# Kernel tuning notes

Measured on AMD Instinct MI355X. Metric: run time of the kernel, lower is better.

The kernel has to match this reference:

```python
import jax, jax.numpy as jnp
import numpy as np

NH, NKV, D = 16, 4, 64
E, NG, TKG, TOPK = 64, 8, 4, 8
RSF = 2.5
EPS = 1e-6
THETA = 10000.0

def rmsnorm(x, w, eps=EPS):
    v = jnp.mean(jnp.square(x.astype(jnp.float32)), axis=-1, keepdims=True)
    return (x * jax.lax.rsqrt(v + eps)).astype(x.dtype) * w

def rope_neox(x, pos):
    # x: [T, heads, D]; neox-style rotation over full head_dim
    d = x.shape[-1]
    inv = 1.0 / (THETA ** (jnp.arange(0, d, 2, dtype=jnp.float32) / d))
    f = pos.astype(jnp.float32)[:, None] * inv              # [T, d/2]
    cos = jnp.cos(f)[:, None, :]
    sin = jnp.sin(f)[:, None, :]
    x1, x2 = jnp.split(x, 2, axis=-1)
    return jnp.concatenate([x1 * cos - x2 * sin, x2 * cos + x1 * sin], axis=-1)


def setup_inputs() -> dict:
    key = jax.random.key(0)
    ks = jax.random.split(key, 12)
    T, H, I, IS = 2048, 1024, 256, 512
    s = 0.02
    return {
        "x": jax.random.normal(ks[0], (T, H), jnp.float32),
        "positions": jnp.arange(T, dtype=jnp.int32),
        "ln1_w": jnp.ones((H,), jnp.float32),
        "w_qkv": jax.random.normal(ks[1], (H, (NH + 2 * NKV) * D), jnp.float32) * s,
        "w_o": jax.random.normal(ks[2], (NH * D, H), jnp.float32) * s,
        "ln2_w": jnp.ones((H,), jnp.float32),
        "gate_w": jax.random.normal(ks[3], (E, H), jnp.float32) * s,
        "expert_bias": jax.random.normal(ks[4], (E,), jnp.float32) * 0.01,
        "we_gate": jax.random.normal(ks[5], (E, H, I), jnp.float32) * s,
        "we_up": jax.random.normal(ks[6], (E, H, I), jnp.float32) * s,
        "we_down": jax.random.normal(ks[7], (E, I, H), jnp.float32) * s,
        "ws_gate_up": jax.random.normal(ks[8], (H, 2 * IS), jnp.float32) * s,
        "ws_down": jax.random.normal(ks[9], (IS, H), jnp.float32) * s,
    }


def reference(x, positions, ln1_w, w_qkv, w_o, ln2_w, gate_w, expert_bias,
              we_gate, we_up, we_down, ws_gate_up, ws_down):
    T, H = x.shape
    residual = x
    # --- attention ---
    h = rmsnorm(x, ln1_w)
    qkv = h @ w_qkv
    q, k, v = jnp.split(qkv, [NH * D, (NH + NKV) * D], axis=-1)
    q = rope_neox(q.reshape(T, NH, D), positions)
    k = rope_neox(k.reshape(T, NKV, D), positions)
    v = v.reshape(T, NKV, D)
    rep = NH // NKV
    k = jnp.repeat(k, rep, axis=1)
    v = jnp.repeat(v, rep, axis=1)
    scores = jnp.einsum('thd,shd->hts', q, k) * (D ** -0.5)
    causal = positions[:, None] >= positions[None, :]
    scores = jnp.where(causal[None], scores, jnp.float32(-1e30))
    p = jax.nn.softmax(scores, axis=-1)
    attn = jnp.einsum('hts,shd->thd', p, v).reshape(T, NH * D)
    residual = residual + attn @ w_o
    # --- MoE block ---
    h = rmsnorm(residual, ln2_w)
    logits = h.astype(jnp.float32) @ gate_w.astype(jnp.float32).T      # [T,E]
    s = jax.nn.sigmoid(logits)
    sc = s + expert_bias[None, :]                                      # bias-corrected scores
    # grouped top-k: score each group by sum of its top-2 corrected scores
    gsc = sc.reshape(T, NG, E // NG)
    group_scores = jax.lax.top_k(gsc, 2)[0].sum(-1)                    # [T,NG]
    _, gidx = jax.lax.top_k(group_scores, TKG)
    gmask = jnp.zeros((T, NG), bool).at[jnp.arange(T)[:, None], gidx].set(True)
    sc_masked = jnp.where(jnp.repeat(gmask, E // NG, axis=1), sc, -jnp.inf)
    _, ids = jax.lax.top_k(sc_masked, TOPK)                            # [T,k]
    w = jnp.take_along_axis(s, ids, axis=-1)                           # weights from raw sigmoid scores
    w = w / (w.sum(-1, keepdims=True) + 1e-20)
    w = w * RSF
    combine = jnp.zeros((T, E), jnp.float32).at[jnp.arange(T)[:, None], ids].add(w)
    combine = combine.astype(h.dtype)
    # routed experts (dense-over-experts reference of the grouped-GEMM dispatch)
    g = jnp.einsum('th,ehi->tei', h, we_gate)
    u = jnp.einsum('th,ehi->tei', h, we_up)
    act = jax.nn.silu(g) * u
    y = jnp.einsum('tei,eih,te->th', act, we_down, combine)
    # shared expert (SwiGLU)
    gu = h @ ws_gate_up
    gs, us = jnp.split(gu, 2, axis=-1)
    y = y + (jax.nn.silu(gs) * us) @ ws_down
    return residual + y
```

## Files before the change

### kernel.cpp

```cpp
#include <hip/hip_runtime.h>
#include <hip/hip_bf16.h>
#include <math.h>

#define T_TOK 2048
#define H_DIM 1024
#define NHH 16
#define NKVH 4
#define HD 64
#define QKV_N 1536
#define NE 64
#define NGRP 8
#define TKG 4
#define TOPKK 8
#define EI 256
#define ISH 512
#define NPOS (T_TOK * TOPKK)

typedef __bf16 bf16_t;
typedef bf16_t bf16x8 __attribute__((ext_vector_type(8)));
typedef bf16_t bf16x4v __attribute__((ext_vector_type(4)));
typedef float f32x4 __attribute__((ext_vector_type(4)));

#define MFMA_BF16 __builtin_amdgcn_mfma_f32_16x16x32_bf16

__global__ void rmsnorm_k(const float* __restrict__ x, const float* __restrict__ w,
                          float* __restrict__ outf, bf16_t* __restrict__ outb) {
  const int t = blockIdx.x;
  const int tid = threadIdx.x;
  const float* xp = x + (size_t)t * H_DIM;
  const float4 x4 = *(const float4*)(xp + tid * 4);
  float s = x4.x * x4.x + x4.y * x4.y + x4.z * x4.z + x4.w * x4.w;
#pragma unroll
  for (int off = 32; off >= 1; off >>= 1) s += __shfl_xor(s, off);
  __shared__ float red[4];
  if ((tid & 63) == 0) red[tid >> 6] = s;
  __syncthreads();
  const float tot = red[0] + red[1] + red[2] + red[3];
  const float r = rsqrtf(tot / (float)H_DIM + 1e-6f);
  const float4 w4 = *(const float4*)(w + tid * 4);
  float4 o;
  o.x = x4.x * r * w4.x; o.y = x4.y * r * w4.y;
  o.z = x4.z * r * w4.z; o.w = x4.w * r * w4.w;
  if (outf) *(float4*)(outf + (size_t)t * H_DIM + tid * 4) = o;
  bf16x4v ob;
  ob[0] = (bf16_t)o.x; ob[1] = (bf16_t)o.y; ob[2] = (bf16_t)o.z; ob[3] = (bf16_t)o.w;
  *(bf16x4v*)(outb + (size_t)t * H_DIM + tid * 4) = ob;
}

__global__ void castT_k(const float* __restrict__ src, bf16_t* __restrict__ dst,
                        int R, int C, size_t srcStride, size_t dstStride,
                        int dstLD, int rowOff) {
  const int e = blockIdx.z;
  const float* sp = src + (size_t)e * srcStride;
  bf16_t* dp = dst + (size_t)e * dstStride;
  const int r0 = blockIdx.y * 32, c0 = blockIdx.x * 32;
  const int tid = threadIdx.x;
  __shared__ float tl[32][33];
  {
    const int rr = tid >> 3, cc4 = (tid & 7) * 4;
    const float4 v = *(const float4*)(sp + (size_t)(r0 + rr) * C + c0 + cc4);
    tl[rr][cc4 + 0] = v.x; tl[rr][cc4 + 1] = v.y;
    tl[rr][cc4 + 2] = v.z; tl[rr][cc4 + 3] = v.w;
  }
  __syncthreads();
  {
    const int cc = tid >> 3, rr4 = (tid & 7) * 4;
    bf16x4v o;
#pragma unroll
    for (int i = 0; i < 4; i++) o[i] = (bf16_t)tl[rr4 + i][cc];
    *(bf16x4v*)(dp + (size_t)(rowOff + c0 + cc) * dstLD + r0 + rr4) = o;
  }
}

__global__ __launch_bounds__(256) void mfma_gemm_k(
    const bf16_t* __restrict__ A, const bf16_t* __restrict__ Bt,
    const float* __restrict__ add0, const float* __restrict__ add1,
    float* __restrict__ C, int M, int N, int K) {
  __shared__ bf16_t Al[128 * 64];
  __shared__ bf16_t Bl[128 * 64];
  const int tid = threadIdx.x;
  const int lane = tid & 63, wave = tid >> 6;
  const int wm = wave >> 1, wn = wave & 1;
  const int lrow = lane & 15, lq = lane >> 4;
  const int m0 = blockIdx.y * 128, n0 = blockIdx.x * 128;
  const int arow = tid >> 1, qb = (tid & 1) * 4;
  const bf16_t* Arow = A + (size_t)(m0 + arow) * K + qb * 8;
  const bf16_t* Brow = Bt + (size_t)(n0 + arow) * K + qb * 8;
  f32x4 acc[4][4];
#pragma unroll
  for (int i = 0; i < 4; i++)
#pragma unroll
    for (int j = 0; j < 4; j++) acc[i][j] = (f32x4){0.f, 0.f, 0.f, 0.f};
  for (int k0 = 0; k0 < K; k0 += 64) {
    __syncthreads();
#pragma unroll
    for (int i = 0; i < 4; i++) {
      const int q = qb + i;
      *(bf16x8*)&Al[(q * 128 + arow) * 8] = *(const bf16x8*)(Arow + k0 + i * 8);
      *(bf16x8*)&Bl[(q * 128 + arow) * 8] = *(const bf16x8*)(Brow + k0 + i * 8);
    }
    __syncthreads();
#pragma unroll
    for (int kb = 0; kb < 2; kb++) {
      bf16x8 af[4], bfr[4];
#pragma unroll
      for (int i = 0; i < 4; i++) {
        af[i]  = *(const bf16x8*)&Al[((kb * 4 + lq) * 128 + wm * 64 + i * 16 + lrow) * 8];
        bfr[i] = *(const bf16x8*)&Bl[((kb * 4 + lq) * 128 + wn * 64 + i * 16 + lrow) * 8];
      }
#pragma unroll
      for (int i = 0; i < 4; i++)
#pragma unroll
        for (int j = 0; j < 4; j++)
          acc[i][j] = MFMA_BF16(af[i], bfr[j], acc[i][j], 0, 0, 0);
    }
  }
#pragma unroll
  for (int i = 0; i < 4; i++)
#pragma unroll
    for (int r = 0; r < 4; r++) {
      const int m = m0 + wm * 64 + i * 16 + lq * 4 + r;
#pragma unroll
      for (int j = 0; j < 4; j++) {
        const int n = n0 + wn * 64 + j * 16 + lrow;
        float v = acc[i][j][r];
        if (add0) v += add0[(size_t)m * N + n];
        if (add1) v += add1[(size_t)m * N + n];
        C[(size_t)m * N + n] = v;
      }
    }
}

__global__ __launch_bounds__(256) void mfma_gateup_k(
    const bf16_t* __restrict__ h2b, const bf16_t* __restrict__ weT,
    const int* __restrict__ ptok, const int* __restrict__ offs,
    bf16_t* __restrict__ gu_e) {
  const int e = blockIdx.z;
  const int base = offs[e];
  const int cnt = offs[e + 1] - base;
  const int m0 = blockIdx.y * 128;
  if (m0 >= cnt) return;
  const int n0 = blockIdx.x * 128;
  __shared__ bf16_t Al[128 * 64];
  __shared__ bf16_t Bl[128 * 64];
  __shared__ int toks[128];
  const int tid = threadIdx.x;
  if (tid < 128) toks[tid] = ptok[base + min(m0 + tid, cnt - 1)];
  const int lane = tid & 63, wave = tid >> 6;
  const int wm = wave >> 1, wn = wave & 1;
  const int lrow = lane & 15, lq = lane >> 4;
  const int arow = tid >> 1, qb = (tid & 1) * 4;
  const bf16_t* Bt = weT + (size_t)e * 512 * 1024;
  const bf16_t* Brow = Bt + (size_t)(n0 + arow) * 1024 + qb * 8;
  f32x4 acc[4][4];
#pragma unroll
  for (int i = 0; i < 4; i++)
#pragma unroll
    for (int j = 0; j < 4; j++) acc[i][j] = (f32x4){0.f, 0.f, 0.f, 0.f};
  for (int k0 = 0; k0 < 1024; k0 += 64) {
    __syncthreads();
    const bf16_t* Arow = h2b + (size_t)toks[arow] * 1024 + qb * 8;
#pragma unroll
    for (int i = 0; i < 4; i++) {
      const int q = qb + i;
      *(bf16x8*)&Al[(q * 128 + arow) * 8] = *(const bf16x8*)(Arow + k0 + i * 8);
      *(bf16x8*)&Bl[(q * 128 + arow) * 8] = *(const bf16x8*)(Brow + k0 + i * 8);
    }
    __syncthreads();
#pragma unroll
    for (int kb = 0; kb < 2; kb++) {
      bf16x8 af[4], bfr[4];
#pragma unroll
      for (int i = 0; i < 4; i++) {
        af[i]  = *(const bf16x8*)&Al[((kb * 4 + lq) * 128 + wm * 64 + i * 16 + lrow) * 8];
        bfr[i] = *(const bf16x8*)&Bl[((kb * 4 + lq) * 128 + wn * 64 + i * 16 + lrow) * 8];
      }
#pragma unroll
      for (int i = 0; i < 4; i++)
#pragma unroll
        for (int j = 0; j < 4; j++)
          acc[i][j] = MFMA_BF16(af[i], bfr[j], acc[i][j], 0, 0, 0);
    }
  }
#pragma unroll
  for (int i = 0; i < 4; i++)
#pragma unroll
    for (int r = 0; r < 4; r++) {
      const int mloc = m0 + wm * 64 + i * 16 + lq * 4 + r;
      if (mloc < cnt) {
#pragma unroll
        for (int j = 0; j < 4; j++) {
          const int n = n0 + wn * 64 + j * 16 + lrow;
          gu_e[(size_t)(base + mloc) * 512 + n] = (bf16_t)acc[i][j][r];
        }
      }
    }
}

__global__ __launch_bounds__(256) void mfma_down_k(
    const bf16_t* __restrict__ actb, const bf16_t* __restrict__ wdT,
    const int* __restrict__ ptok, const float* __restrict__ pw,
    const int* __restrict__ offs, float* __restrict__ y) {
  const int e = blockIdx.z;
  const int base = offs[e];
  const int cnt = offs[e + 1] - base;
  const int m0 = blockIdx.y * 128;
  if (m0 >= cnt) return;
  const int n0 = blockIdx.x * 128;
  __shared__ bf16_t Al[128 * 64];
  __shared__ bf16_t Bl[128 * 64];
  const int tid = threadIdx.x;
  const int lane = tid & 63, wave = tid >> 6;
  const int wm = wave >> 1, wn = wave & 1;
  const int lrow = lane & 15, lq = lane >> 4;
  const int arow = tid >> 1, qb = (tid & 1) * 4;
  const int agrow = base + min(m0 + arow, cnt - 1);
  const bf16_t* Arow = actb + (size_t)agrow * 256 + qb * 8;
  const bf16_t* Brow = wdT + (size_t)e * 1024 * 256 + (size_t)(n0 + arow) * 256 + qb * 8;
  f32x4 acc[4][4];
#pragma unroll
  for (int i = 0; i < 4; i++)
#pragma unroll
    for (int j = 0; j < 4; j++) acc[i][j] = (f32x4){0.f, 0.f, 0.f, 0.f};
  for (int k0 = 0; k0 < 256; k0 += 64) {
    __syncthreads();
#pragma unroll
    for (int i = 0; i < 4; i++) {
      const int q = qb + i;
      *(bf16x8*)&Al[(q * 128 + arow) * 8] = *(const bf16x8*)(Arow + k0 + i * 8);
      *(bf16x8*)&Bl[(q * 128 + arow) * 8] = *(const bf16x8*)(Brow + k0 + i * 8);
    }
    __syncthreads();
#pragma unroll
    for (int kb = 0; kb < 2; kb++) {
      bf16x8 af[4], bfr[4];
#pragma unroll
      for (int i = 0; i < 4; i++) {
        af[i]  = *(const bf16x8*)&Al[((kb * 4 + lq) * 128 + wm * 64 + i * 16 + lrow) * 8];
        bfr[i] = *(const bf16x8*)&Bl[((kb * 4 + lq) * 128 + wn * 64 + i * 16 + lrow) * 8];
      }
#pragma unroll
      for (int i = 0; i < 4; i++)
#pragma unroll
        for (int j = 0; j < 4; j++)
          acc[i][j] = MFMA_BF16(af[i], bfr[j], acc[i][j], 0, 0, 0);
    }
  }
#pragma unroll
  for (int i = 0; i < 4; i++)
#pragma unroll
    for (int r = 0; r < 4; r++) {
      const int mloc = m0 + wm * 64 + i * 16 + lq * 4 + r;
      if (mloc < cnt) {
        const float wv = pw[base + mloc];
        const int tok = ptok[base + mloc];
#pragma unroll
        for (int j = 0; j < 4; j++) {
          const int n = n0 + wn * 64 + j * 16 + lrow;
          atomicAdd(&y[(size_t)tok * H_DIM + n], wv * acc[i][j][r]);
        }
      }
    }
}

__global__ void rope_k(float* __restrict__ qkv, const int* __restrict__ positions) {
  const int t = blockIdx.x, h = blockIdx.y;
  const int i = threadIdx.x;
  const float inv = exp2f((float)i * (-13.287712379549449f / 32.0f));
  const float f = (float)positions[t] * inv;
  float sn, c;
  sincosf(f, &sn, &c);
  float* p = qkv + (size_t)t * QKV_N + h * HD;
  const float x1 = p[i], x2 = p[i + 32];
  p[i] = x1 * c - x2 * sn;
  p[i + 32] = x2 * c + x1 * sn;
}

__global__ __launch_bounds__(256) void attn_k(const float* __restrict__ qkv,
                                              bf16_t* __restrict__ attnb) {
  const int qt = (T_TOK / 64 - 1) - blockIdx.x;
  const int h = blockIdx.y;
  const int g = h >> 2;
  const int tid = threadIdx.x;
  const int tx = tid & 15, ty = tid >> 4;
  __shared__ float Qt[64][68];
  __shared__ float Kd[64][68];
  __shared__ float Vt[64][68];
  {
    const int i = tid & 63, dg = tid >> 6;
    const float* qp = qkv + (size_t)(qt * 64 + i) * QKV_N + h * HD;
#pragma unroll
    for (int r = 0; r < 4; r++) {
      const int d = dg * 16 + r * 4;
      const float4 v = *(const float4*)(qp + d);
      Qt[d + 0][i] = v.x * 0.125f;
      Qt[d + 1][i] = v.y * 0.125f;
      Qt[d + 2][i] = v.z * 0.125f;
      Qt[d + 3][i] = v.w * 0.125f;
    }
  }
  float m[4], l[4], acc[4][4];
#pragma unroll
  for (int i = 0; i < 4; i++) {
    m[i] = -1e30f; l[i] = 0.f;
#pragma unroll
    for (int j = 0; j < 4; j++) acc[i][j] = 0.f;
  }
  const float* kbase = qkv + NHH * HD + g * HD;
  const float* vbase = qkv + (NHH + NKVH) * HD + g * HD;
  const int jj_stage = tid & 63, dg_stage = tid >> 6;
  for (int s0 = 0; s0 <= qt * 64; s0 += 64) {
    __syncthreads();
    {
      const float* kp = kbase + (size_t)(s0 + jj_stage) * QKV_N;
      const float* vp = vbase + (size_t)(s0 + jj_stage) * QKV_N;
#pragma unroll
      for (int r = 0; r < 4; r++) {
        const int d = dg_stage * 16 + r * 4;
        const float4 k4 = *(const float4*)(kp + d);
        Kd[d + 0][jj_stage] = k4.x; Kd[d + 1][jj_stage] = k4.y;
        Kd[d + 2][jj_stage] = k4.z; Kd[d + 3][jj_stage] = k4.w;
        *(float4*)&Vt[jj_stage][d] = *(const float4*)(vp + d);
      }
    }
    __syncthreads();
    float s[4][4] = {};
#pragma unroll 8
    for (int d = 0; d < 64; d++) {
      const float4 a = *(const float4*)&Qt[d][ty << 2];
      const float4 b = *(const float4*)&Kd[d][tx << 2];
      const float ar[4] = {a.x, a.y, a.z, a.w};
      const float br[4] = {b.x, b.y, b.z, b.w};
#pragma unroll
      for (int i = 0; i < 4; i++)
#pragma unroll
        for (int j = 0; j < 4; j++) s[i][j] += ar[i] * br[j];
    }
    if (s0 == qt * 64) {
#pragma unroll
      for (int i = 0; i < 4; i++)
#pragma unroll
        for (int j = 0; j < 4; j++)
          if ((tx << 2) + j > (ty << 2) + i) s[i][j] = -1e30f;
    }
#pragma unroll
    for (int i = 0; i < 4; i++) {
      float mx = fmaxf(fmaxf(s[i][0], s[i][1]), fmaxf(s[i][2], s[i][3]));
#pragma unroll
      for (int off = 1; off <= 8; off <<= 1) mx = fmaxf(mx, __shfl_xor(mx, off));
      const float mnew = fmaxf(m[i], mx);
      const float alpha = expf(m[i] - mnew);
      float ps = 0.f;
#pragma unroll
      for (int j = 0; j < 4; j++) { const float p = expf(s[i][j] - mnew); s[i][j] = p; ps += p; }
#pragma unroll
      for (int off = 1; off <= 8; off <<= 1) ps += __shfl_xor(ps, off);
      l[i] = l[i] * alpha + ps;
      m[i] = mnew;
#pragma unroll
      for (int j = 0; j < 4; j++) acc[i][j] *= alpha;
    }
    __syncthreads();
#pragma unroll
    for (int i = 0; i < 4; i++)
#pragma unroll
      for (int j = 0; j < 4; j++) Kd[(tx << 2) + j][(ty << 2) + i] = s[i][j];
    __syncthreads();
#pragma unroll 8
    for (int jj = 0; jj < 64; jj++) {
      const float4 a = *(const float4*)&Kd[jj][ty << 2];
      const float4 b = *(const float4*)&Vt[jj][tx << 2];
      const float ar[4] = {a.x, a.y, a.z, a.w};
      const float br[4] = {b.x, b.y, b.z, b.w};
#pragma unroll
      for (int i = 0; i < 4; i++)
#pragma unroll
        for (int j = 0; j < 4; j++) acc[i][j] += ar[i] * br[j];
    }
  }
#pragma unroll
  for (int i = 0; i < 4; i++) {
    const int t = qt * 64 + (ty << 2) + i;
    const float invl = 1.f / l[i];
    bf16x4v o;
    o[0] = (bf16_t)(acc[i][0] * invl); o[1] = (bf16_t)(acc[i][1] * invl);
    o[2] = (bf16_t)(acc[i][2] * invl); o[3] = (bf16_t)(acc[i][3] * invl);
    *(bf16x4v*)(attnb + (size_t)t * (NHH * HD) + h * HD + (tx << 2)) = o;
  }
}

__global__ void gate_logits_k(const float* __restrict__ h2, const float* __restrict__ gw,
                              float* __restrict__ logits) {
  const int t = blockIdx.x;
  const int e = threadIdx.x;
  const float* hp = h2 + (size_t)t * H_DIM;
  const float* gp = gw + (size_t)e * H_DIM;
  float s = 0.f;
  for (int i = 0; i < H_DIM; i += 4) {
    const float4 h4 = *(const float4*)(hp + i);
    const float4 g4 = *(const float4*)(gp + i);
    s += h4.x * g4.x + h4.y * g4.y + h4.z * g4.z + h4.w * g4.w;
  }
  logits[t * NE + e] = s;
}

__global__ void route_k(const float* __restrict__ logits, const float* __restrict__ ebias,
                        int* __restrict__ topk_ids, float* __restrict__ topk_w) {
  const int t = blockIdx.x * 64 + threadIdx.x;
  if (t >= T_TOK) return;
  float s[NE], sc[NE];
  const float* lp = logits + t * NE;
#pragma unroll
  for (int e = 0; e < NE; e++) {
    const float v = 1.f / (1.f + expf(-lp[e]));
    s[e] = v;
    sc[e] = v + ebias[e];
  }
  float gsc[NGRP];
#pragma unroll
  for (int gi = 0; gi < NGRP; gi++) {
    float m1 = -1e30f, m2 = -1e30f;
#pragma unroll
    for (int j = 0; j < 8; j++) {
      const float v = sc[gi * 8 + j];
      if (v > m1) { m2 = m1; m1 = v; } else if (v > m2) m2 = v;
    }
    gsc[gi] = m1 + m2;
  }
  unsigned gmask = 0;
  for (int k2 = 0; k2 < TKG; k2++) {
    int bi = 0; float b = -3.4e38f;
#pragma unroll
    for (int gi = 0; gi < NGRP; gi++)
      if (!((gmask >> gi) & 1u) && gsc[gi] > b) { b = gsc[gi]; bi = gi; }
    gmask |= 1u << bi;
  }
  unsigned long long esel = 0ull;
  float wsum = 0.f;
  int ids[TOPKK]; float wv[TOPKK];
  for (int k2 = 0; k2 < TOPKK; k2++) {
    int bi = 0; float b = -3.4e38f;
    for (int e = 0; e < NE; e++) {
      if (((gmask >> (e >> 3)) & 1u) && !((esel >> e) & 1ull) && sc[e] > b) { b = sc[e]; bi = e; }
    }
    esel |= 1ull << bi;
    ids[k2] = bi;
    wv[k2] = s[bi];
    wsum += wv[k2];
  }
  const float norm = 2.5f / (wsum + 1e-20f);
#pragma unroll
  for (int k2 = 0; k2 < TOPKK; k2++) {
    topk_ids[t * TOPKK + k2] = ids[k2];
    topk_w[t * TOPKK + k2] = wv[k2] * norm;
  }
}

__global__ void count_k(const int* __restrict__ ids, int* __restrict__ counts) {
  const int idx = blockIdx.x * 256 + threadIdx.x;
  if (idx < NPOS) atomicAdd(&counts[ids[idx]], 1);
}

__global__ void offsets_k(const int* __restrict__ counts, int* __restrict__ offsets,
                          int* __restrict__ cursor) {
  if (threadIdx.x == 0 && blockIdx.x == 0) {
    int acc = 0;
    for (int e = 0; e < NE; e++) { offsets[e] = acc; cursor[e] = acc; acc += counts[e]; }
    offsets[NE] = acc;
  }
}

__global__ void scatter_k(const int* __restrict__ ids, const float* __restrict__ wts,
                          int* __restrict__ cursor, int* __restrict__ perm_tok,
                          float* __restrict__ perm_w) {
  const int idx = blockIdx.x * 256 + threadIdx.x;
  if (idx >= NPOS) return;
  const int e = ids[idx];
  const int pos = atomicAdd(&cursor[e], 1);
  perm_tok[pos] = idx >> 3;
  perm_w[pos] = wts[idx];
}

__global__ void act2_k(const bf16_t* __restrict__ gu_e, bf16_t* __restrict__ actb) {
  const int row = blockIdx.x;
  const int c = threadIdx.x;
  const float g = (float)gu_e[(size_t)row * 512 + c];
  const float u = (float)gu_e[(size_t)row * 512 + 256 + c];
  actb[(size_t)row * 256 + c] = (bf16_t)(g / (1.f + expf(-g)) * u);
}

__global__ void sact_k(const float* __restrict__ gu, bf16_t* __restrict__ sa) {
  const int idx = blockIdx.x * 256 + threadIdx.x;
  const int t = idx >> 9, i = idx & 511;
  const float g = gu[(size_t)t * 1024 + i];
  const float u = gu[(size_t)t * 1024 + 512 + i];
  sa[idx] = (bf16_t)(g / (1.f + expf(-g)) * u);
}

extern "C" void kernel_launch(void* const* d_in, const int* in_sizes, int n_in,
                              void* d_out, int out_size, void* d_ws, size_t ws_size,
                              hipStream_t stream) {
  const float* x         = (const float*)d_in[0];
  const int*   positions = (const int*)d_in[1];
  const float* ln1_w     = (const float*)d_in[2];
  const float* w_qkv     = (const float*)d_in[3];
  const float* w_o       = (const float*)d_in[4];
  const float* ln2_w     = (const float*)d_in[5];
  const float* gate_w    = (const float*)d_in[6];
  const float* ebias     = (const float*)d_in[7];
  const float* we_gate   = (const float*)d_in[8];
  const float* we_up     = (const float*)d_in[9];
  const float* we_down   = (const float*)d_in[10];
  const float* ws_gateup = (const float*)d_in[11];
  const float* ws_down   = (const float*)d_in[12];
  float* out = (float*)d_out;

  char* wsp = (char*)d_ws;
  size_t off = 0;
  auto alloc = [&](size_t bytes) {
    void* p = wsp + off;
    off += (bytes + 255) & ~(size_t)255;
    return p;
  };
  float*  qkv    = (float*)alloc((size_t)T_TOK * QKV_N * 4);
  bf16_t* attnb  = (bf16_t*)alloc((size_t)T_TOK * H_DIM * 2);
  bf16_t* gu_e   = (bf16_t*)qkv;
  bf16_t* h1b    = (bf16_t*)alloc((size_t)T_TOK * H_DIM * 2);
  bf16_t* sa     = h1b;
  float*  resid1 = (float*)alloc((size_t)T_TOK * H_DIM * 4);
  float*  h2f    = (float*)alloc((size_t)T_TOK * H_DIM * 4);
  bf16_t* h2b    = (bf16_t*)alloc((size_t)T_TOK * H_DIM * 2);
  float*  logits = (float*)alloc((size_t)T_TOK * NE * 4);
  int*    tids   = (int*)alloc((size_t)NPOS * 4);
  float*  tw     = (float*)alloc((size_t)NPOS * 4);
  int*    counts = (int*)alloc(NE * 4);
  int*    offs   = (int*)alloc((NE + 1) * 4);
  int*    cursor = (int*)alloc(NE * 4);
  int*    ptok   = (int*)alloc((size_t)NPOS * 4);
  float*  pw     = (float*)alloc((size_t)NPOS * 4);
  bf16_t* actb   = (bf16_t*)alloc((size_t)NPOS * EI * 2);
  float*  y      = (float*)alloc((size_t)T_TOK * H_DIM * 4);
  float*  gu     = (float*)alloc((size_t)T_TOK * 1024 * 4);
  bf16_t* wqkvT  = (bf16_t*)alloc((size_t)QKV_N * H_DIM * 2);
  bf16_t* woT    = (bf16_t*)alloc((size_t)H_DIM * H_DIM * 2);
  bf16_t* wsguT  = (bf16_t*)alloc((size_t)1024 * H_DIM * 2);
  bf16_t* wsdT   = (bf16_t*)alloc((size_t)H_DIM * ISH * 2);
  bf16_t* weT    = (bf16_t*)alloc((size_t)NE * 512 * H_DIM * 2);
  bf16_t* wdT    = (bf16_t*)alloc((size_t)NE * H_DIM * EI * 2);
  (void)ws_size; (void)in_sizes; (void)n_in; (void)out_size;

  castT_k<<<dim3(QKV_N / 32, H_DIM / 32, 1), 256, 0, stream>>>(
      w_qkv, wqkvT, H_DIM, QKV_N, 0, 0, H_DIM, 0);
  castT_k<<<dim3(H_DIM / 32, H_DIM / 32, 1), 256, 0, stream>>>(
      w_o, woT, H_DIM, H_DIM, 0, 0, H_DIM, 0);
  castT_k<<<dim3(1024 / 32, H_DIM / 32, 1), 256, 0, stream>>>(
      ws_gateup, wsguT, H_DIM, 1024, 0, 0, H_DIM, 0);
  castT_k<<<dim3(H_DIM / 32, ISH / 32, 1), 256, 0, stream>>>(
      ws_down, wsdT, ISH, H_DIM, 0, 0, ISH, 0);
  castT_k<<<dim3(EI / 32, H_DIM / 32, NE), 256, 0, stream>>>(
      we_gate, weT, H_DIM, EI, (size_t)H_DIM * EI, (size_t)512 * H_DIM, H_DIM, 0);
  castT_k<<<dim3(EI / 32, H_DIM / 32, NE), 256, 0, stream>>>(
      we_up, weT, H_DIM, EI, (size_t)H_DIM * EI, (size_t)512 * H_DIM, H_DIM, 256);
  castT_k<<<dim3(H_DIM / 32, EI / 32, NE), 256, 0, stream>>>(
      we_down, wdT, EI, H_DIM, (size_t)EI * H_DIM, (size_t)H_DIM * EI, EI, 0);

  hipMemsetAsync(counts, 0, NE * 4, stream);
  hipMemsetAsync(y, 0, (size_t)T_TOK * H_DIM * 4, stream);

  rmsnorm_k<<<T_TOK, 256, 0, stream>>>(x, ln1_w, nullptr, h1b);
  mfma_gemm_k<<<dim3(QKV_N / 128, T_TOK / 128), 256, 0, stream>>>(
      h1b, wqkvT, nullptr, nullptr, qkv, T_TOK, QKV_N, H_DIM);
  rope_k<<<dim3(T_TOK, NHH + NKVH), 32, 0, stream>>>(qkv, positions);
  attn_k<<<dim3(T_TOK / 64, NHH), 256, 0, stream>>>(qkv, attnb);
  mfma_gemm_k<<<dim3(H_DIM / 128, T_TOK / 128), 256, 0, stream>>>(
      attnb, woT, x, nullptr, resid1, T_TOK, H_DIM, H_DIM);

  rmsnorm_k<<<T_TOK, 256, 0, stream>>>(resid1, ln2_w, h2f, h2b);
  gate_logits_k<<<T_TOK, 64, 0, stream>>>(h2f, gate_w, logits);
  route_k<<<T_TOK / 64, 64, 0, stream>>>(logits, ebias, tids, tw);
  count_k<<<NPOS / 256, 256, 0, stream>>>(tids, counts);
  offsets_k<<<1, 1, 0, stream>>>(counts, offs, cursor);
  scatter_k<<<NPOS / 256, 256, 0, stream>>>(tids, tw, cursor, ptok, pw);

  mfma_gateup_k<<<dim3(512 / 128, T_TOK / 128, NE), 256, 0, stream>>>(
      h2b, weT, ptok, offs, gu_e);
  act2_k<<<NPOS, 256, 0, stream>>>(gu_e, actb);
  mfma_down_k<<<dim3(H_DIM / 128, T_TOK / 128, NE), 256, 0, stream>>>(
      actb, wdT, ptok, pw, offs, y);

  mfma_gemm_k<<<dim3(1024 / 128, T_TOK / 128), 256, 0, stream>>>(
      h2b, wsguT, nullptr, nullptr, gu, T_TOK, 1024, H_DIM);
  sact_k<<<(T_TOK * ISH) / 256, 256, 0, stream>>>(gu, sa);
  mfma_gemm_k<<<dim3(H_DIM / 128, T_TOK / 128), 256, 0, stream>>>(
      sa, wsdT, resid1, y, out, T_TOK, H_DIM, ISH);
}
```

Measured before the change: 998.4 us.

## Move attention QK and PV products onto bf16 MFMA with split-precision emulation

Rewrites the causal attention kernel to compute QK^T and PV with 16x16x32 bf16 MFMA instructions instead of scalar FP32 FMAs. Each operand is split into a bf16 high part and a bf16 residual, and three MFMAs per product approximate FP32 accuracy. K, V and P are staged in LDS as bf16 with a rotated layout for V to avoid bank conflicts. The grid is reordered so heads vary fastest, which lets blocks sharing a KV group run close together and reuse K/V in cache. The cost is extra conversion work and three MFMAs per product, plus a small loss of precision relative to full FP32.

```diff
diff --git a/kernel.cpp b/kernel.cpp
--- a/kernel.cpp
+++ b/kernel.cpp
@@ -278,114 +278,167 @@
 
 __global__ __launch_bounds__(256) void attn_k(const float* __restrict__ qkv,
                                               bf16_t* __restrict__ attnb) {
-  const int qt = (T_TOK / 64 - 1) - blockIdx.x;
-  const int h = blockIdx.y;
+  const int h = blockIdx.x;
+  const int qt = (T_TOK / 64 - 1) - blockIdx.y;
   const int g = h >> 2;
   const int tid = threadIdx.x;
-  const int tx = tid & 15, ty = tid >> 4;
-  __shared__ float Qt[64][68];
-  __shared__ float Kd[64][68];
-  __shared__ float Vt[64][68];
+  const int lane = tid & 63, wave = tid >> 6;
+  const int lcol = lane & 15, lk = lane >> 4;
+
+  __shared__ bf16_t Kh[64][72];
+  __shared__ bf16_t Ko[64][72];
+  __shared__ bf16_t Vh[64][72];
+  __shared__ bf16_t Vl[64][72];
+  __shared__ bf16_t Ph[64][72];
+  __shared__ bf16_t Po[64][72];
+
+  bf16x8 aqh[2], aql[2];
   {
-    const int i = tid & 63, dg = tid >> 6;
-    const float* qp = qkv + (size_t)(qt * 64 + i) * QKV_N + h * HD;
-#pragma unroll
-    for (int r = 0; r < 4; r++) {
-      const int d = dg * 16 + r * 4;
-      const float4 v = *(const float4*)(qp + d);
-      Qt[d + 0][i] = v.x * 0.125f;
-      Qt[d + 1][i] = v.y * 0.125f;
-      Qt[d + 2][i] = v.z * 0.125f;
-      Qt[d + 3][i] = v.w * 0.125f;
-    }
-  }
-  float m[4], l[4], acc[4][4];
-#pragma unroll
-  for (int i = 0; i < 4; i++) {
-    m[i] = -1e30f; l[i] = 0.f;
-#pragma unroll
-    for (int j = 0; j < 4; j++) acc[i][j] = 0.f;
-  }
+    const int qrow = qt * 64 + wave * 16 + lcol;
+    const float* qp = qkv + (size_t)qrow * QKV_N + h * HD + lk * 8;
+#pragma unroll
+    for (int ks = 0; ks < 2; ks++) {
+      const float4 a = *(const float4*)(qp + ks * 32);
+      const float4 b = *(const float4*)(qp + ks * 32 + 4);
+      const float qv[8] = {a.x, a.y, a.z, a.w, b.x, b.y, b.z, b.w};
+#pragma unroll
+      for (int j = 0; j < 8; j++) {
+        const float v = qv[j] * 0.125f;
+        const bf16_t hi = (bf16_t)v;
+        aqh[ks][j] = hi;
+        aql[ks][j] = (bf16_t)(v - (float)hi);
+      }
+    }
+  }
+
+  float m[4], l[4];
+  f32x4 acc[4];
+#pragma unroll
+  for (int r = 0; r < 4; r++) { m[r] = -1e30f; l[r] = 0.f; }
+#pragma unroll
+  for (int n = 0; n < 4; n++) acc[n] = (f32x4){0.f, 0.f, 0.f, 0.f};
+
   const float* kbase = qkv + NHH * HD + g * HD;
   const float* vbase = qkv + (NHH + NKVH) * HD + g * HD;
-  const int jj_stage = tid & 63, dg_stage = tid >> 6;
+  const int srow = tid >> 2;
+  const int scb = tid & 3;
+
   for (int s0 = 0; s0 <= qt * 64; s0 += 64) {
     __syncthreads();
     {
-      const float* kp = kbase + (size_t)(s0 + jj_stage) * QKV_N;
-      const float* vp = vbase + (size_t)(s0 + jj_stage) * QKV_N;
+      const float* kp = kbase + (size_t)(s0 + srow) * QKV_N + scb * 16;
+      const float* vp = vbase + (size_t)(s0 + srow) * QKV_N + scb * 16;
+      const float4 k0 = *(const float4*)(kp + 0);
+      const float4 k1 = *(const float4*)(kp + 4);
+      const float4 k2 = *(const float4*)(kp + 8);
+      const float4 k3 = *(const float4*)(kp + 12);
+      const float kv[16] = {k0.x, k0.y, k0.z, k0.w, k1.x, k1.y, k1.z, k1.w,
+                            k2.x, k2.y, k2.z, k2.w, k3.x, k3.y, k3.z, k3.w};
+      bf16x8 h0, h1, o0, o1;
+#pragma unroll
+      for (int j = 0; j < 8; j++) {
+        const bf16_t hi = (bf16_t)kv[j];
+        h0[j] = hi; o0[j] = (bf16_t)(kv[j] - (float)hi);
+        const bf16_t hi2 = (bf16_t)kv[j + 8];
+        h1[j] = hi2; o1[j] = (bf16_t)(kv[j + 8] - (float)hi2);
+      }
+      *(bf16x8*)&Kh[srow][scb * 16] = h0;
+      *(bf16x8*)&Kh[srow][scb * 16 + 8] = h1;
+      *(bf16x8*)&Ko[srow][scb * 16] = o0;
+      *(bf16x8*)&Ko[srow][scb * 16 + 8] = o1;
+      const float4 v0 = *(const float4*)(vp + 0);
+      const float4 v1 = *(const float4*)(vp + 4);
+      const float4 v2 = *(const float4*)(vp + 8);
+      const float4 v3 = *(const float4*)(vp + 12);
+      const float vv[16] = {v0.x, v0.y, v0.z, v0.w, v1.x, v1.y, v1.z, v1.w,
+                            v2.x, v2.y, v2.z, v2.w, v3.x, v3.y, v3.z, v3.w};
+#pragma unroll
+      for (int r2 = 0; r2 < 16; r2++) {
+        const int d = scb * 16 + r2;
+        const int col = (srow + (d & 56)) & 63;
+        const bf16_t hi = (bf16_t)vv[r2];
+        Vh[d][col] = hi;
+        Vl[d][col] = (bf16_t)(vv[r2] - (float)hi);
+      }
+    }
+    __syncthreads();
+    f32x4 s4[4];
+#pragma unroll
+    for (int n = 0; n < 4; n++) s4[n] = (f32x4){0.f, 0.f, 0.f, 0.f};
+#pragma unroll
+    for (int ks = 0; ks < 2; ks++) {
+#pragma unroll
+      for (int n = 0; n < 4; n++) {
+        const bf16x8 bh = *(const bf16x8*)&Kh[n * 16 + lcol][ks * 32 + lk * 8];
+        const bf16x8 bo = *(const bf16x8*)&Ko[n * 16 + lcol][ks * 32 + lk * 8];
+        s4[n] = MFMA_BF16(aqh[ks], bh, s4[n], 0, 0, 0);
+        s4[n] = MFMA_BF16(aqh[ks], bo, s4[n], 0, 0, 0);
+        s4[n] = MFMA_BF16(aql[ks], bh, s4[n], 0, 0, 0);
+      }
+    }
+    if (s0 == qt * 64) {
+#pragma unroll
+      for (int n = 0; n < 4; n++) {
+        const int col = n * 16 + lcol;
+#pragma unroll
+        for (int r = 0; r < 4; r++)
+          if (col > wave * 16 + lk * 4 + r) s4[n][r] = -1e30f;
+      }
+    }
+#pragma unroll
+    for (int r = 0; r < 4; r++) {
+      float mx = fmaxf(fmaxf(s4[0][r], s4[1][r]), fmaxf(s4[2][r], s4[3][r]));
+#pragma unroll
+      for (int off = 1; off <= 8; off <<= 1) mx = fmaxf(mx, __shfl_xor(mx, off));
+      const float mnew = fmaxf(m[r], mx);
+      const float alpha = expf(m[r] - mnew);
+      float ps = 0.f;
+#pragma unroll
+      for (int n = 0; n < 4; n++) {
+        const float p = expf(s4[n][r] - mnew);
+        s4[n][r] = p; ps += p;
+      }
+#pragma unroll
+      for (int off = 1; off <= 8; off <<= 1) ps += __shfl_xor(ps, off);
+      l[r] = l[r] * alpha + ps;
+      m[r] = mnew;
+#pragma unroll
+      for (int n = 0; n < 4; n++) acc[n][r] *= alpha;
+    }
+#pragma unroll
+    for (int n = 0; n < 4; n++)
 #pragma unroll
       for (int r = 0; r < 4; r++) {
-        const int d = dg_stage * 16 + r * 4;
-        const float4 k4 = *(const float4*)(kp + d);
-        Kd[d + 0][jj_stage] = k4.x; Kd[d + 1][jj_stage] = k4.y;
-        Kd[d + 2][jj_stage] = k4.z; Kd[d + 3][jj_stage] = k4.w;
-        *(float4*)&Vt[jj_stage][d] = *(const float4*)(vp + d);
-      }
-    }
-    __syncthreads();
-    float s[4][4] = {};
-#pragma unroll 8
-    for (int d = 0; d < 64; d++) {
-      const float4 a = *(const float4*)&Qt[d][ty << 2];
-      const float4 b = *(const float4*)&Kd[d][tx << 2];
-      const float ar[4] = {a.x, a.y, a.z, a.w};
-      const float br[4] = {b.x, b.y, b.z, b.w};
-#pragma unroll
-      for (int i = 0; i < 4; i++)
-#pragma unroll
-        for (int j = 0; j < 4; j++) s[i][j] += ar[i] * br[j];
-    }
-    if (s0 == qt * 64) {
-#pragma unroll
-      for (int i = 0; i < 4; i++)
-#pragma unroll
-        for (int j = 0; j < 4; j++)
-          if ((tx << 2) + j > (ty << 2) + i) s[i][j] = -1e30f;
-    }
-#pragma unroll
-    for (int i = 0; i < 4; i++) {
-      float mx = fmaxf(fmaxf(s[i][0], s[i][1]), fmaxf(s[i][2], s[i][3]));
-#pragma unroll
-      for (int off = 1; off <= 8; off <<= 1) mx = fmaxf(mx, __shfl_xor(mx, off));
-      const float mnew = fmaxf(m[i], mx);
-      const float alpha = expf(m[i] - mnew);
-      float ps = 0.f;
-#pragma unroll
-      for (int j = 0; j < 4; j++) { const float p = expf(s[i][j] - mnew); s[i][j] = p; ps += p; }
-#pragma unroll
-      for (int off = 1; off <= 8; off <<= 1) ps += __shfl_xor(ps, off);
-      l[i] = l[i] * alpha + ps;
-      m[i] = mnew;
-#pragma unroll
-      for (int j = 0; j < 4; j++) acc[i][j] *= alpha;
-    }
-    __syncthreads();
-#pragma unroll
-    for (int i = 0; i < 4; i++)
-#pragma unroll
-      for (int j = 0; j < 4; j++) Kd[(tx << 2) + j][(ty << 2) + i] = s[i][j];
-    __syncthreads();
-#pragma unroll 8
-    for (int jj = 0; jj < 64; jj++) {
-      const float4 a = *(const float4*)&Kd[jj][ty << 2];
-      const float4 b = *(const float4*)&Vt[jj][tx << 2];
-      const float ar[4] = {a.x, a.y, a.z, a.w};
-      const float br[4] = {b.x, b.y, b.z, b.w};
-#pragma unroll
-      for (int i = 0; i < 4; i++)
-#pragma unroll
-        for (int j = 0; j < 4; j++) acc[i][j] += ar[i] * br[j];
-    }
-  }
-#pragma unroll
-  for (int i = 0; i < 4; i++) {
-    const int t = qt * 64 + (ty << 2) + i;
-    const float invl = 1.f / l[i];
-    bf16x4v o;
-    o[0] = (bf16_t)(acc[i][0] * invl); o[1] = (bf16_t)(acc[i][1] * invl);
-    o[2] = (bf16_t)(acc[i][2] * invl); o[3] = (bf16_t)(acc[i][3] * invl);
-    *(bf16x4v*)(attnb + (size_t)t * (NHH * HD) + h * HD + (tx << 2)) = o;
+        const float p = s4[n][r];
+        const bf16_t hi = (bf16_t)p;
+        Ph[wave * 16 + lk * 4 + r][n * 16 + lcol] = hi;
+        Po[wave * 16 + lk * 4 + r][n * 16 + lcol] = (bf16_t)(p - (float)hi);
+      }
+    __syncthreads();
+#pragma unroll
+    for (int ks = 0; ks < 2; ks++) {
+      const bf16x8 pah = *(const bf16x8*)&Ph[wave * 16 + lcol][ks * 32 + lk * 8];
+      const bf16x8 pao = *(const bf16x8*)&Po[wave * 16 + lcol][ks * 32 + lk * 8];
+#pragma unroll
+      for (int n = 0; n < 4; n++) {
+        const int d = n * 16 + lcol;
+        const int c0 = (ks * 32 + lk * 8 + (d & 56)) & 63;
+        const bf16x8 bvh = *(const bf16x8*)&Vh[d][c0];
+        const bf16x8 bvl = *(const bf16x8*)&Vl[d][c0];
+        acc[n] = MFMA_BF16(pah, bvh, acc[n], 0, 0, 0);
+        acc[n] = MFMA_BF16(pah, bvl, acc[n], 0, 0, 0);
+        acc[n] = MFMA_BF16(pao, bvh, acc[n], 0, 0, 0);
+      }
+    }
+  }
+#pragma unroll
+  for (int r = 0; r < 4; r++) {
+    const int trow = qt * 64 + wave * 16 + lk * 4 + r;
+    const float invl = 1.f / l[r];
+#pragma unroll
+    for (int n = 0; n < 4; n++)
+      attnb[(size_t)trow * (NHH * HD) + h * HD + n * 16 + lcol] =
+          (bf16_t)(acc[n][r] * invl);
   }
 }
 
@@ -571,7 +624,7 @@
   mfma_gemm_k<<<dim3(QKV_N / 128, T_TOK / 128), 256, 0, stream>>>(
       h1b, wqkvT, nullptr, nullptr, qkv, T_TOK, QKV_N, H_DIM);
   rope_k<<<dim3(T_TOK, NHH + NKVH), 32, 0, stream>>>(qkv, positions);
-  attn_k<<<dim3(T_TOK / 64, NHH), 256, 0, stream>>>(qkv, attnb);
+  attn_k<<<dim3(NHH, T_TOK / 64), 256, 0, stream>>>(qkv, attnb);
   mfma_gemm_k<<<dim3(H_DIM / 128, T_TOK / 128), 256, 0, stream>>>(
       attnb, woT, x, nullptr, resid1, T_TOK, H_DIM, H_DIM);
 
```

Measured after the change: 827.6 us. -17.1%, faster.
